# Optimization experiments

Hardware: AMD Instinct MI355X
Metric: run time of the kernel (lower is better)

## Reference

```python
import jax, jax.numpy as jnp
import numpy as np

N, D, K = 131072, 64, 1024


def setup_inputs() -> dict:
    key = jax.random.key(0)
    kx, kc = jax.random.split(key)
    x = jax.random.normal(kx, (N, D), dtype=jnp.float32)
    codebook = jax.random.normal(kc, (K, D), dtype=jnp.float32)
    return {"x": x, "codebook": codebook}


def reference(x, codebook):
    # Pairwise squared L2 distances, expanded form to avoid the [N, K, D]
    # intermediate the naive vmap would materialize:
    x_sq = jnp.sum(x * x, axis=-1, keepdims=True)            # [N, 1]
    c_sq = jnp.sum(codebook * codebook, axis=-1)             # [K]
    xc = jnp.einsum("nd,kd->nk", x, codebook)                # [N, K]
    l2_sum = x_sq - 2.0 * xc + c_sq[None, :]                 # [N, K]
    codes = jnp.argmin(l2_sum, axis=-1)                      # [N] int
    code_vec = jnp.take(codebook, codes, axis=0)             # [N, D]
    return (code_vec, codes, l2_sum)
```

## Files before the change

### kernel.cpp

```cpp
#include <hip/hip_runtime.h>
#include <stdint.h>

#define NROWS 131072
#define DDIM  64
#define KCB   1024
#define BM    128
#define NCHUNK 16
#define XPAD  68

typedef short bf16x8 __attribute__((ext_vector_type(8)));
typedef float f32x4  __attribute__((ext_vector_type(4)));

__device__ __forceinline__ unsigned short f2bf(float f) {
    unsigned int u = __float_as_uint(f);
    u += 0x7FFFu + ((u >> 16) & 1u);
    return (unsigned short)(u >> 16);
}
__device__ __forceinline__ float bf2f(unsigned short h) {
    return __uint_as_float(((unsigned int)h) << 16);
}

__global__ __launch_bounds__(256)
void convert_cb(const float* __restrict__ cb,
                unsigned short* __restrict__ mh,
                unsigned short* __restrict__ ml,
                float* __restrict__ csq) {
    const int t    = blockIdx.x * 256 + threadIdx.x;
    const int row  = t >> 2;
    const int part = t & 3;
    const float4* src = (const float4*)(cb + (size_t)row * DDIM + part * 16);

    unsigned short hb[16], lb[16];
    float s = 0.f;
#pragma unroll
    for (int q = 0; q < 4; ++q) {
        float4 v = src[q];
        float c, m; unsigned short h;
        c = v.x; s = fmaf(c, c, s); m = -2.f * c; h = f2bf(m);
        hb[q*4+0] = h; lb[q*4+0] = f2bf(m - bf2f(h));
        c = v.y; s = fmaf(c, c, s); m = -2.f * c; h = f2bf(m);
        hb[q*4+1] = h; lb[q*4+1] = f2bf(m - bf2f(h));
        c = v.z; s = fmaf(c, c, s); m = -2.f * c; h = f2bf(m);
        hb[q*4+2] = h; lb[q*4+2] = f2bf(m - bf2f(h));
        c = v.w; s = fmaf(c, c, s); m = -2.f * c; h = f2bf(m);
        hb[q*4+3] = h; lb[q*4+3] = f2bf(m - bf2f(h));
    }
    s += __shfl_xor(s, 1);
    s += __shfl_xor(s, 2);
    if (part == 0) csq[row] = s;

    const size_t off = (size_t)row * DDIM + part * 16;
    short4* dh = (short4*)(mh + off);
    short4* dl = (short4*)(ml + off);
#pragma unroll
    for (int q = 0; q < 4; ++q) {
        short4 hv, lv;
        hv.x = (short)hb[q*4+0]; hv.y = (short)hb[q*4+1];
        hv.z = (short)hb[q*4+2]; hv.w = (short)hb[q*4+3];
        lv.x = (short)lb[q*4+0]; lv.y = (short)lb[q*4+1];
        lv.z = (short)lb[q*4+2]; lv.w = (short)lb[q*4+3];
        dh[q] = hv; dl[q] = lv;
    }
}

__device__ __forceinline__ void cvt8(float4 f0, float4 f1, bf16x8* h, bf16x8* l) {
    bf16x8 hh, ll;
    float fv; unsigned short hb;
    fv = f0.x; hb = f2bf(fv); hh[0] = (short)hb; ll[0] = (short)f2bf(fv - bf2f(hb));
    fv = f0.y; hb = f2bf(fv); hh[1] = (short)hb; ll[1] = (short)f2bf(fv - bf2f(hb));
    fv = f0.z; hb = f2bf(fv); hh[2] = (short)hb; ll[2] = (short)f2bf(fv - bf2f(hb));
    fv = f0.w; hb = f2bf(fv); hh[3] = (short)hb; ll[3] = (short)f2bf(fv - bf2f(hb));
    fv = f1.x; hb = f2bf(fv); hh[4] = (short)hb; ll[4] = (short)f2bf(fv - bf2f(hb));
    fv = f1.y; hb = f2bf(fv); hh[5] = (short)hb; ll[5] = (short)f2bf(fv - bf2f(hb));
    fv = f1.z; hb = f2bf(fv); hh[6] = (short)hb; ll[6] = (short)f2bf(fv - bf2f(hb));
    fv = f1.w; hb = f2bf(fv); hh[7] = (short)hb; ll[7] = (short)f2bf(fv - bf2f(hb));
    *h = hh; *l = ll;
}

__global__ __launch_bounds__(256, 4)
void codebook_mfma(const float* __restrict__ x,
                   const float* __restrict__ cb,
                   const unsigned short* __restrict__ cbh,
                   const unsigned short* __restrict__ cbl,
                   const float* __restrict__ csq,
                   float* __restrict__ out_codevec,
                   float* __restrict__ out_codes,
                   float* __restrict__ out_l2) {
    __shared__ float xs[BM][XPAD];
    __shared__ float xsq_s[BM];
    __shared__ int   cand_s[BM][2];

    const int tid  = threadIdx.x;
    const int lane = tid & 63;
    const int wid  = tid >> 6;
    const int row0 = blockIdx.x * BM;

    {
        const int r = tid >> 1, h = tid & 1;
        const float4* src = (const float4*)(x + (size_t)(row0 + r) * DDIM + h * 32);
        float4* dst = (float4*)&xs[r][h * 32];
        float s0 = 0.f, s1 = 0.f;
#pragma unroll
        for (int q = 0; q < 8; ++q) {
            float4 v = src[q];
            dst[q] = v;
            s0 = fmaf(v.x, v.x, s0); s0 = fmaf(v.y, v.y, s0);
            s1 = fmaf(v.z, v.z, s1); s1 = fmaf(v.w, v.w, s1);
        }
        float s = s0 + s1;
        s += __shfl_xor(s, 1);
        if (h == 0) xsq_s[r] = s;
    }
    __syncthreads();

    const int mrow = wid * 32;
    const int cl   = lane & 15;
    const int ch   = lane >> 4;

    bf16x8 xh[2][2], xl[2][2];
#pragma unroll
    for (int mt = 0; mt < 2; ++mt)
#pragma unroll
    for (int ks = 0; ks < 2; ++ks) {
        const float* p = &xs[mrow + mt * 16 + cl][ks * 32 + ch * 8];
        cvt8(*(const float4*)p, *(const float4*)(p + 4), &xh[mt][ks], &xl[mt][ks]);
    }

    float xq[2];
    xq[0] = xsq_s[mrow + cl];
    xq[1] = xsq_s[mrow + 16 + cl];

    float m1[2], m2[2];
    int   i1[2], i2[2];
#pragma unroll
    for (int mt = 0; mt < 2; ++mt) {
        m1[mt] = 3.4e38f; m2[mt] = 3.4e38f; i1[mt] = 0; i2[mt] = 0;
    }

    for (int chunk = 0; chunk < NCHUNK; ++chunk) {
        const int k0 = chunk << 6;

#pragma unroll
        for (int nt = 0; nt < 4; ++nt) {
            const int ncol = k0 + nt * 16 + cl;
            const size_t bof = (size_t)ncol * DDIM + ch * 8;
            const bf16x8 bh0 = *(const bf16x8*)(cbh + bof);
            const bf16x8 bh1 = *(const bf16x8*)(cbh + bof + 32);
            const bf16x8 bl0 = *(const bf16x8*)(cbl + bof);
            const bf16x8 bl1 = *(const bf16x8*)(cbl + bof + 32);
            const f32x4  cqv = *(const f32x4*)(csq + k0 + nt * 16 + ch * 4);

#pragma unroll
            for (int mt = 0; mt < 2; ++mt) {
                f32x4 a;
                a[0] = xq[mt] + cqv[0]; a[1] = xq[mt] + cqv[1];
                a[2] = xq[mt] + cqv[2]; a[3] = xq[mt] + cqv[3];
                a = __builtin_amdgcn_mfma_f32_16x16x32_bf16(bh0, xh[mt][0], a, 0, 0, 0);
                a = __builtin_amdgcn_mfma_f32_16x16x32_bf16(bh1, xh[mt][1], a, 0, 0, 0);
                a = __builtin_amdgcn_mfma_f32_16x16x32_bf16(bh0, xl[mt][0], a, 0, 0, 0);
                a = __builtin_amdgcn_mfma_f32_16x16x32_bf16(bh1, xl[mt][1], a, 0, 0, 0);
                a = __builtin_amdgcn_mfma_f32_16x16x32_bf16(bl0, xh[mt][0], a, 0, 0, 0);
                a = __builtin_amdgcn_mfma_f32_16x16x32_bf16(bl1, xh[mt][1], a, 0, 0, 0);

                f32x4* dst = (f32x4*)(out_l2 +
                    (size_t)(row0 + mrow + mt * 16 + cl) * KCB + k0 + nt * 16 + ch * 4);
                *dst = a;

                const int idx0 = k0 + nt * 16 + ch * 4;
#pragma unroll
                for (int rg = 0; rg < 4; ++rg) {
                    const float v = a[rg];
                    const int idx = idx0 + rg;
                    const bool c1 = v < m1[mt];
                    const bool c2 = v < m2[mt];
                    const float nm2 = c1 ? m1[mt] : (c2 ? v : m2[mt]);
                    const int   ni2 = c1 ? i1[mt] : (c2 ? idx : i2[mt]);
                    m2[mt] = nm2; i2[mt] = ni2;
                    m1[mt] = c1 ? v : m1[mt];
                    i1[mt] = c1 ? idx : i1[mt];
                }
            }
        }
    }

#pragma unroll
    for (int mt = 0; mt < 2; ++mt) {
        float a1 = m1[mt], a2 = m2[mt];
        int   j1 = i1[mt], j2 = i2[mt];
#pragma unroll
        for (int mm = 16; mm <= 32; mm <<= 1) {
            float o1 = __shfl_xor(a1, mm), o2 = __shfl_xor(a2, mm);
            int   q1 = __shfl_xor(j1, mm), q2 = __shfl_xor(j2, mm);
            const bool fw = (o1 < a1) || (o1 == a1 && q1 < j1);
            const float w1 = fw ? o1 : a1; const int wj1 = fw ? q1 : j1;
            const float ca = fw ? a1 : o1; const int cja = fw ? j1 : q1;
            const float cbv = fw ? o2 : a2; const int cjb = fw ? q2 : j2;
            const bool sw = (cbv < ca) || (cbv == ca && cjb < cja);
            a1 = w1; j1 = wj1;
            a2 = sw ? cbv : ca; j2 = sw ? cjb : cja;
        }
        if (ch == 0) {
            const int r = mrow + mt * 16 + cl;
            cand_s[r][0] = j1; cand_s[r][1] = j2;
        }
    }
    __syncthreads();

    {
        const int r = tid >> 1, h = tid & 1;
        const int cand = cand_s[r][h];
        const float4* xr = (const float4*)&xs[r][0];
        const float4* cr = (const float4*)(cb + (size_t)cand * DDIM);
        float s0 = 0.f, s1 = 0.f, s2 = 0.f, s3 = 0.f;
#pragma unroll
        for (int q = 0; q < 4; ++q) {
            float4 xa, ca;
            xa = xr[q];      ca = cr[q];
            s0 = fmaf(xa.x, ca.x, s0); s0 = fmaf(xa.y, ca.y, s0);
            s0 = fmaf(xa.z, ca.z, s0); s0 = fmaf(xa.w, ca.w, s0);
            xa = xr[q + 4];  ca = cr[q + 4];
            s1 = fmaf(xa.x, ca.x, s1); s1 = fmaf(xa.y, ca.y, s1);
            s1 = fmaf(xa.z, ca.z, s1); s1 = fmaf(xa.w, ca.w, s1);
            xa = xr[q + 8];  ca = cr[q + 8];
            s2 = fmaf(xa.x, ca.x, s2); s2 = fmaf(xa.y, ca.y, s2);
            s2 = fmaf(xa.z, ca.z, s2); s2 = fmaf(xa.w, ca.w, s2);
            xa = xr[q + 12]; ca = cr[q + 12];
            s3 = fmaf(xa.x, ca.x, s3); s3 = fmaf(xa.y, ca.y, s3);
            s3 = fmaf(xa.z, ca.z, s3); s3 = fmaf(xa.w, ca.w, s3);
        }
        const float dot = (s0 + s1) + (s2 + s3);
        const float d = fmaf(-2.f, dot, xsq_s[r] + csq[cand]);
        const float od = __shfl_xor(d, 1);
        const int   oc = __shfl_xor(cand, 1);
        const bool win = (d < od) || (d == od && cand < oc);
        const int w = win ? cand : oc;
        if (h == 0) out_codes[row0 + r] = (float)w;
        const float4* wv = (const float4*)(cb + (size_t)w * DDIM + h * 32);
        float4* ov = (float4*)(out_codevec + (size_t)(row0 + r) * DDIM + h * 32);
#pragma unroll
        for (int q = 0; q < 8; ++q) ov[q] = wv[q];
    }
}

extern "C" void kernel_launch(void* const* d_in, const int* in_sizes, int n_in,
                              void* d_out, int out_size, void* d_ws, size_t ws_size,
                              hipStream_t stream) {
    (void)in_sizes; (void)n_in; (void)out_size; (void)ws_size;
    const float* x  = (const float*)d_in[0];
    const float* cb = (const float*)d_in[1];

    unsigned short* cbh = (unsigned short*)d_ws;
    unsigned short* cbl = cbh + (size_t)KCB * DDIM;
    float*          csq = (float*)(cbl + (size_t)KCB * DDIM);

    float* out_codevec = (float*)d_out;
    float* out_codes   = out_codevec + (size_t)NROWS * DDIM;
    float* out_l2      = out_codes + NROWS;

    convert_cb<<<16, 256, 0, stream>>>(cb, cbh, cbl, csq);
    codebook_mfma<<<NROWS / BM, 256, 0, stream>>>(x, cb, cbh, cbl, csq,
                                                  out_codevec, out_codes, out_l2);
}
```

Measured before the change: 256.8 us.

## Halve row tile per block and batch L2 stores per 256-column group

Shrinks the block tile from 128 to 64 rows so each wave handles a single 16-row MFMA tile, which doubles the number of blocks while each block still reads the full codebook. Accumulators for 256 codebook columns are held in registers and written to the L2 output in a burst after each group instead of right after each tile's MFMAs. The epilogue is respread over four threads per row. The aim is more parallelism and better-grouped output stores, at the cost of twice the codebook reads per row and higher register pressure, with occupancy lowered to 3 waves in launch bounds.

```diff
diff --git a/kernel.cpp b/kernel.cpp
--- a/kernel.cpp
+++ b/kernel.cpp
@@ -4,8 +4,7 @@
 #define NROWS 131072
 #define DDIM  64
 #define KCB   1024
-#define BM    128
-#define NCHUNK 16
+#define BM    64
 #define XPAD  68
 
 typedef short bf16x8 __attribute__((ext_vector_type(8)));
@@ -77,7 +76,7 @@
     *h = hh; *l = ll;
 }
 
-__global__ __launch_bounds__(256, 4)
+__global__ __launch_bounds__(256, 3)
 void codebook_mfma(const float* __restrict__ x,
                    const float* __restrict__ cb,
                    const unsigned short* __restrict__ cbh,
@@ -96,12 +95,12 @@
     const int row0 = blockIdx.x * BM;
 
     {
-        const int r = tid >> 1, h = tid & 1;
-        const float4* src = (const float4*)(x + (size_t)(row0 + r) * DDIM + h * 32);
-        float4* dst = (float4*)&xs[r][h * 32];
+        const int r = tid >> 2, p = tid & 3;
+        const float4* src = (const float4*)(x + (size_t)(row0 + r) * DDIM + p * 16);
+        float4* dst = (float4*)&xs[r][p * 16];
         float s0 = 0.f, s1 = 0.f;
 #pragma unroll
-        for (int q = 0; q < 8; ++q) {
+        for (int q = 0; q < 4; ++q) {
             float4 v = src[q];
             dst[q] = v;
             s0 = fmaf(v.x, v.x, s0); s0 = fmaf(v.y, v.y, s0);
@@ -109,84 +108,84 @@
         }
         float s = s0 + s1;
         s += __shfl_xor(s, 1);
-        if (h == 0) xsq_s[r] = s;
+        s += __shfl_xor(s, 2);
+        if (p == 0) xsq_s[r] = s;
     }
     __syncthreads();
 
-    const int mrow = wid * 32;
+    const int wrow = wid * 16;
     const int cl   = lane & 15;
     const int ch   = lane >> 4;
 
-    bf16x8 xh[2][2], xl[2][2];
-#pragma unroll
-    for (int mt = 0; mt < 2; ++mt)
+    bf16x8 xh[2], xl[2];
 #pragma unroll
     for (int ks = 0; ks < 2; ++ks) {
-        const float* p = &xs[mrow + mt * 16 + cl][ks * 32 + ch * 8];
-        cvt8(*(const float4*)p, *(const float4*)(p + 4), &xh[mt][ks], &xl[mt][ks]);
-    }
-
-    float xq[2];
-    xq[0] = xsq_s[mrow + cl];
-    xq[1] = xsq_s[mrow + 16 + cl];
-
-    float m1[2], m2[2];
-    int   i1[2], i2[2];
-#pragma unroll
-    for (int mt = 0; mt < 2; ++mt) {
-        m1[mt] = 3.4e38f; m2[mt] = 3.4e38f; i1[mt] = 0; i2[mt] = 0;
-    }
-
-    for (int chunk = 0; chunk < NCHUNK; ++chunk) {
-        const int k0 = chunk << 6;
-
-#pragma unroll
-        for (int nt = 0; nt < 4; ++nt) {
-            const int ncol = k0 + nt * 16 + cl;
-            const size_t bof = (size_t)ncol * DDIM + ch * 8;
-            const bf16x8 bh0 = *(const bf16x8*)(cbh + bof);
-            const bf16x8 bh1 = *(const bf16x8*)(cbh + bof + 32);
-            const bf16x8 bl0 = *(const bf16x8*)(cbl + bof);
-            const bf16x8 bl1 = *(const bf16x8*)(cbl + bof + 32);
-            const f32x4  cqv = *(const f32x4*)(csq + k0 + nt * 16 + ch * 4);
-
-#pragma unroll
-            for (int mt = 0; mt < 2; ++mt) {
+        const float* p = &xs[wrow + cl][ks * 32 + ch * 8];
+        cvt8(*(const float4*)p, *(const float4*)(p + 4), &xh[ks], &xl[ks]);
+    }
+    const float xq = xsq_s[wrow + cl];
+
+    float m1 = 3.4e38f, m2 = 3.4e38f;
+    int   i1 = 0, i2 = 0;
+
+    const size_t rowbase = (size_t)(row0 + wrow + cl) * KCB;
+
+#pragma unroll
+    for (int g = 0; g < 4; ++g) {
+        f32x4 acc[4][4];
+
+#pragma unroll
+        for (int c = 0; c < 4; ++c) {
+            const int k0 = (g * 4 + c) << 6;
+#pragma unroll
+            for (int nt = 0; nt < 4; ++nt) {
+                const int ncol = k0 + nt * 16 + cl;
+                const size_t bof = (size_t)ncol * DDIM + ch * 8;
+                const bf16x8 bh0 = *(const bf16x8*)(cbh + bof);
+                const bf16x8 bh1 = *(const bf16x8*)(cbh + bof + 32);
+                const bf16x8 bl0 = *(const bf16x8*)(cbl + bof);
+                const bf16x8 bl1 = *(const bf16x8*)(cbl + bof + 32);
+                const f32x4  cqv = *(const f32x4*)(csq + k0 + nt * 16 + ch * 4);
+
                 f32x4 a;
-                a[0] = xq[mt] + cqv[0]; a[1] = xq[mt] + cqv[1];
-                a[2] = xq[mt] + cqv[2]; a[3] = xq[mt] + cqv[3];
-                a = __builtin_amdgcn_mfma_f32_16x16x32_bf16(bh0, xh[mt][0], a, 0, 0, 0);
-                a = __builtin_amdgcn_mfma_f32_16x16x32_bf16(bh1, xh[mt][1], a, 0, 0, 0);
-                a = __builtin_amdgcn_mfma_f32_16x16x32_bf16(bh0, xl[mt][0], a, 0, 0, 0);
-                a = __builtin_amdgcn_mfma_f32_16x16x32_bf16(bh1, xl[mt][1], a, 0, 0, 0);
-                a = __builtin_amdgcn_mfma_f32_16x16x32_bf16(bl0, xh[mt][0], a, 0, 0, 0);
-                a = __builtin_amdgcn_mfma_f32_16x16x32_bf16(bl1, xh[mt][1], a, 0, 0, 0);
-
-                f32x4* dst = (f32x4*)(out_l2 +
-                    (size_t)(row0 + mrow + mt * 16 + cl) * KCB + k0 + nt * 16 + ch * 4);
-                *dst = a;
+                a[0] = xq + cqv[0]; a[1] = xq + cqv[1];
+                a[2] = xq + cqv[2]; a[3] = xq + cqv[3];
+                a = __builtin_amdgcn_mfma_f32_16x16x32_bf16(bh0, xh[0], a, 0, 0, 0);
+                a = __builtin_amdgcn_mfma_f32_16x16x32_bf16(bh1, xh[1], a, 0, 0, 0);
+                a = __builtin_amdgcn_mfma_f32_16x16x32_bf16(bh0, xl[0], a, 0, 0, 0);
+                a = __builtin_amdgcn_mfma_f32_16x16x32_bf16(bh1, xl[1], a, 0, 0, 0);
+                a = __builtin_amdgcn_mfma_f32_16x16x32_bf16(bl0, xh[0], a, 0, 0, 0);
+                a = __builtin_amdgcn_mfma_f32_16x16x32_bf16(bl1, xh[1], a, 0, 0, 0);
+                acc[c][nt] = a;
 
                 const int idx0 = k0 + nt * 16 + ch * 4;
 #pragma unroll
                 for (int rg = 0; rg < 4; ++rg) {
                     const float v = a[rg];
                     const int idx = idx0 + rg;
-                    const bool c1 = v < m1[mt];
-                    const bool c2 = v < m2[mt];
-                    const float nm2 = c1 ? m1[mt] : (c2 ? v : m2[mt]);
-                    const int   ni2 = c1 ? i1[mt] : (c2 ? idx : i2[mt]);
-                    m2[mt] = nm2; i2[mt] = ni2;
-                    m1[mt] = c1 ? v : m1[mt];
-                    i1[mt] = c1 ? idx : i1[mt];
+                    const bool c1 = v < m1;
+                    const bool c2 = v < m2;
+                    const float nm2 = c1 ? m1 : (c2 ? v : m2);
+                    const int   ni2 = c1 ? i1 : (c2 ? idx : i2);
+                    m2 = nm2; i2 = ni2;
+                    m1 = c1 ? v : m1;
+                    i1 = c1 ? idx : i1;
                 }
             }
         }
-    }
-
-#pragma unroll
-    for (int mt = 0; mt < 2; ++mt) {
-        float a1 = m1[mt], a2 = m2[mt];
-        int   j1 = i1[mt], j2 = i2[mt];
+
+#pragma unroll
+        for (int c = 0; c < 4; ++c)
+#pragma unroll
+        for (int nt = 0; nt < 4; ++nt) {
+            f32x4* dst = (f32x4*)(out_l2 + rowbase + g * 256 + c * 64 + nt * 16 + ch * 4);
+            *dst = acc[c][nt];
+        }
+    }
+
+    {
+        float a1 = m1, a2 = m2;
+        int   j1 = i1, j2 = i2;
 #pragma unroll
         for (int mm = 16; mm <= 32; mm <<= 1) {
             float o1 = __shfl_xor(a1, mm), o2 = __shfl_xor(a2, mm);
@@ -200,45 +199,41 @@
             a2 = sw ? cbv : ca; j2 = sw ? cjb : cja;
         }
         if (ch == 0) {
-            const int r = mrow + mt * 16 + cl;
-            cand_s[r][0] = j1; cand_s[r][1] = j2;
+            cand_s[wrow + cl][0] = j1; cand_s[wrow + cl][1] = j2;
         }
     }
     __syncthreads();
 
     {
-        const int r = tid >> 1, h = tid & 1;
-        const int cand = cand_s[r][h];
-        const float4* xr = (const float4*)&xs[r][0];
-        const float4* cr = (const float4*)(cb + (size_t)cand * DDIM);
-        float s0 = 0.f, s1 = 0.f, s2 = 0.f, s3 = 0.f;
+        const int r = tid >> 2, p = tid & 3;
+        const int half = p & 1;
+        const int cnd  = p >> 1;
+        const int cand = cand_s[r][cnd];
+        const float4* xr = (const float4*)&xs[r][half * 32];
+        const float4* cr = (const float4*)(cb + (size_t)cand * DDIM + half * 32);
+        float s0 = 0.f, s1 = 0.f;
 #pragma unroll
         for (int q = 0; q < 4; ++q) {
             float4 xa, ca;
-            xa = xr[q];      ca = cr[q];
+            xa = xr[q];     ca = cr[q];
             s0 = fmaf(xa.x, ca.x, s0); s0 = fmaf(xa.y, ca.y, s0);
             s0 = fmaf(xa.z, ca.z, s0); s0 = fmaf(xa.w, ca.w, s0);
-            xa = xr[q + 4];  ca = cr[q + 4];
+            xa = xr[q + 4]; ca = cr[q + 4];
             s1 = fmaf(xa.x, ca.x, s1); s1 = fmaf(xa.y, ca.y, s1);
             s1 = fmaf(xa.z, ca.z, s1); s1 = fmaf(xa.w, ca.w, s1);
-            xa = xr[q + 8];  ca = cr[q + 8];
-            s2 = fmaf(xa.x, ca.x, s2); s2 = fmaf(xa.y, ca.y, s2);
-            s2 = fmaf(xa.z, ca.z, s2); s2 = fmaf(xa.w, ca.w, s2);
-            xa = xr[q + 12]; ca = cr[q + 12];
-            s3 = fmaf(xa.x, ca.x, s3); s3 = fmaf(xa.y, ca.y, s3);
-            s3 = fmaf(xa.z, ca.z, s3); s3 = fmaf(xa.w, ca.w, s3);
-        }
-        const float dot = (s0 + s1) + (s2 + s3);
+        }
+        float dot = s0 + s1;
+        dot += __shfl_xor(dot, 1);
         const float d = fmaf(-2.f, dot, xsq_s[r] + csq[cand]);
-        const float od = __shfl_xor(d, 1);
-        const int   oc = __shfl_xor(cand, 1);
+        const float od = __shfl_xor(d, 2);
+        const int   oc = __shfl_xor(cand, 2);
         const bool win = (d < od) || (d == od && cand < oc);
         const int w = win ? cand : oc;
-        if (h == 0) out_codes[row0 + r] = (float)w;
-        const float4* wv = (const float4*)(cb + (size_t)w * DDIM + h * 32);
-        float4* ov = (float4*)(out_codevec + (size_t)(row0 + r) * DDIM + h * 32);
-#pragma unroll
-        for (int q = 0; q < 8; ++q) ov[q] = wv[q];
+        if (p == 0) out_codes[row0 + r] = (float)w;
+        const float4* wv = (const float4*)(cb + (size_t)w * DDIM + p * 16);
+        float4* ov = (float4*)(out_codevec + (size_t)(row0 + r) * DDIM + p * 16);
+#pragma unroll
+        for (int q = 0; q < 4; ++q) ov[q] = wv[q];
     }
 }
 
```

Result: slower. 308.9 us (+20.3%).

## Double-buffer codebook register loads with sched barriers to overlap MFMA compute

Applied to the files above, without the earlier changes.

Restructures the main loop into 32 steps of 32 codebook columns and uses two register buffers (A/B) so the codebook hi/lo and c_sq loads for the next step are issued before computing the current one. Scheduling barriers pin this order so the compiler cannot merge loads and compute. The aim is to hide global/L2 load latency behind MFMA and argmin work. Doubling the register buffers raises VGPR use, so launch bounds drop from 4 to 3 blocks per SM, which costs occupancy.

```diff
diff --git a/kernel.cpp b/kernel.cpp
--- a/kernel.cpp
+++ b/kernel.cpp
@@ -5,7 +5,7 @@
 #define DDIM  64
 #define KCB   1024
 #define BM    128
-#define NCHUNK 16
+#define NSTEP 32
 #define XPAD  68
 
 typedef short bf16x8 __attribute__((ext_vector_type(8)));
@@ -77,7 +77,67 @@
     *h = hh; *l = ll;
 }
 
-__global__ __launch_bounds__(256, 4)
+__device__ __forceinline__ void prefetch_step(
+        int hh, int cl, int ch,
+        const unsigned short* __restrict__ cbh,
+        const unsigned short* __restrict__ cbl,
+        const float* __restrict__ csq,
+        bf16x8 (&bh0)[2], bf16x8 (&bh1)[2],
+        bf16x8 (&bl0)[2], bf16x8 (&bl1)[2], f32x4 (&cq)[2]) {
+#pragma unroll
+    for (int nt2 = 0; nt2 < 2; ++nt2) {
+        const int ncol = hh * 32 + nt2 * 16 + cl;
+        const size_t bof = (size_t)ncol * DDIM + ch * 8;
+        bh0[nt2] = *(const bf16x8*)(cbh + bof);
+        bh1[nt2] = *(const bf16x8*)(cbh + bof + 32);
+        bl0[nt2] = *(const bf16x8*)(cbl + bof);
+        bl1[nt2] = *(const bf16x8*)(cbl + bof + 32);
+        cq[nt2]  = *(const f32x4*)(csq + hh * 32 + nt2 * 16 + ch * 4);
+    }
+}
+
+__device__ __forceinline__ void compute_step(
+        int hh, int cl, int ch, size_t outbase0, size_t outbase1,
+        const bf16x8 (&bh0)[2], const bf16x8 (&bh1)[2],
+        const bf16x8 (&bl0)[2], const bf16x8 (&bl1)[2], const f32x4 (&cq)[2],
+        const bf16x8 (&xh)[2][2], const bf16x8 (&xl)[2][2], const float (&xq)[2],
+        float (&m1)[2], float (&m2)[2], int (&i1)[2], int (&i2)[2],
+        float* __restrict__ out_l2) {
+#pragma unroll
+    for (int nt2 = 0; nt2 < 2; ++nt2) {
+#pragma unroll
+        for (int mt = 0; mt < 2; ++mt) {
+            f32x4 a;
+            a[0] = xq[mt] + cq[nt2][0]; a[1] = xq[mt] + cq[nt2][1];
+            a[2] = xq[mt] + cq[nt2][2]; a[3] = xq[mt] + cq[nt2][3];
+            a = __builtin_amdgcn_mfma_f32_16x16x32_bf16(bh0[nt2], xh[mt][0], a, 0, 0, 0);
+            a = __builtin_amdgcn_mfma_f32_16x16x32_bf16(bh1[nt2], xh[mt][1], a, 0, 0, 0);
+            a = __builtin_amdgcn_mfma_f32_16x16x32_bf16(bh0[nt2], xl[mt][0], a, 0, 0, 0);
+            a = __builtin_amdgcn_mfma_f32_16x16x32_bf16(bh1[nt2], xl[mt][1], a, 0, 0, 0);
+            a = __builtin_amdgcn_mfma_f32_16x16x32_bf16(bl0[nt2], xh[mt][0], a, 0, 0, 0);
+            a = __builtin_amdgcn_mfma_f32_16x16x32_bf16(bl1[nt2], xh[mt][1], a, 0, 0, 0);
+
+            const int coff = hh * 32 + nt2 * 16 + ch * 4;
+            f32x4* dst = (f32x4*)(out_l2 + (mt == 0 ? outbase0 : outbase1) + coff);
+            *dst = a;
+
+#pragma unroll
+            for (int rg = 0; rg < 4; ++rg) {
+                const float v = a[rg];
+                const int idx = coff + rg;
+                const bool c1 = v < m1[mt];
+                const bool c2 = v < m2[mt];
+                const float nm2 = c1 ? m1[mt] : (c2 ? v : m2[mt]);
+                const int   ni2 = c1 ? i1[mt] : (c2 ? idx : i2[mt]);
+                m2[mt] = nm2; i2[mt] = ni2;
+                m1[mt] = c1 ? v : m1[mt];
+                i1[mt] = c1 ? idx : i1[mt];
+            }
+        }
+    }
+}
+
+__global__ __launch_bounds__(256, 3)
 void codebook_mfma(const float* __restrict__ x,
                    const float* __restrict__ cb,
                    const unsigned short* __restrict__ cbh,
@@ -137,50 +197,28 @@
         m1[mt] = 3.4e38f; m2[mt] = 3.4e38f; i1[mt] = 0; i2[mt] = 0;
     }
 
-    for (int chunk = 0; chunk < NCHUNK; ++chunk) {
-        const int k0 = chunk << 6;
-
-#pragma unroll
-        for (int nt = 0; nt < 4; ++nt) {
-            const int ncol = k0 + nt * 16 + cl;
-            const size_t bof = (size_t)ncol * DDIM + ch * 8;
-            const bf16x8 bh0 = *(const bf16x8*)(cbh + bof);
-            const bf16x8 bh1 = *(const bf16x8*)(cbh + bof + 32);
-            const bf16x8 bl0 = *(const bf16x8*)(cbl + bof);
-            const bf16x8 bl1 = *(const bf16x8*)(cbl + bof + 32);
-            const f32x4  cqv = *(const f32x4*)(csq + k0 + nt * 16 + ch * 4);
-
-#pragma unroll
-            for (int mt = 0; mt < 2; ++mt) {
-                f32x4 a;
-                a[0] = xq[mt] + cqv[0]; a[1] = xq[mt] + cqv[1];
-                a[2] = xq[mt] + cqv[2]; a[3] = xq[mt] + cqv[3];
-                a = __builtin_amdgcn_mfma_f32_16x16x32_bf16(bh0, xh[mt][0], a, 0, 0, 0);
-                a = __builtin_amdgcn_mfma_f32_16x16x32_bf16(bh1, xh[mt][1], a, 0, 0, 0);
-                a = __builtin_amdgcn_mfma_f32_16x16x32_bf16(bh0, xl[mt][0], a, 0, 0, 0);
-                a = __builtin_amdgcn_mfma_f32_16x16x32_bf16(bh1, xl[mt][1], a, 0, 0, 0);
-                a = __builtin_amdgcn_mfma_f32_16x16x32_bf16(bl0, xh[mt][0], a, 0, 0, 0);
-                a = __builtin_amdgcn_mfma_f32_16x16x32_bf16(bl1, xh[mt][1], a, 0, 0, 0);
-
-                f32x4* dst = (f32x4*)(out_l2 +
-                    (size_t)(row0 + mrow + mt * 16 + cl) * KCB + k0 + nt * 16 + ch * 4);
-                *dst = a;
-
-                const int idx0 = k0 + nt * 16 + ch * 4;
-#pragma unroll
-                for (int rg = 0; rg < 4; ++rg) {
-                    const float v = a[rg];
-                    const int idx = idx0 + rg;
-                    const bool c1 = v < m1[mt];
-                    const bool c2 = v < m2[mt];
-                    const float nm2 = c1 ? m1[mt] : (c2 ? v : m2[mt]);
-                    const int   ni2 = c1 ? i1[mt] : (c2 ? idx : i2[mt]);
-                    m2[mt] = nm2; i2[mt] = ni2;
-                    m1[mt] = c1 ? v : m1[mt];
-                    i1[mt] = c1 ? idx : i1[mt];
-                }
-            }
-        }
+    const size_t outbase0 = (size_t)(row0 + mrow + cl) * KCB;
+    const size_t outbase1 = (size_t)(row0 + mrow + 16 + cl) * KCB;
+
+    bf16x8 Abh0[2], Abh1[2], Abl0[2], Abl1[2]; f32x4 Acq[2];
+    bf16x8 Bbh0[2], Bbh1[2], Bbl0[2], Bbl1[2]; f32x4 Bcq[2];
+
+    prefetch_step(0, cl, ch, cbh, cbl, csq, Abh0, Abh1, Abl0, Abl1, Acq);
+
+    for (int h = 0; h < NSTEP; h += 2) {
+        prefetch_step(h + 1, cl, ch, cbh, cbl, csq, Bbh0, Bbh1, Bbl0, Bbl1, Bcq);
+        __builtin_amdgcn_sched_barrier(0);
+        compute_step(h, cl, ch, outbase0, outbase1,
+                     Abh0, Abh1, Abl0, Abl1, Acq,
+                     xh, xl, xq, m1, m2, i1, i2, out_l2);
+        __builtin_amdgcn_sched_barrier(0);
+        if (h + 2 < NSTEP)
+            prefetch_step(h + 2, cl, ch, cbh, cbl, csq, Abh0, Abh1, Abl0, Abl1, Acq);
+        __builtin_amdgcn_sched_barrier(0);
+        compute_step(h + 1, cl, ch, outbase0, outbase1,
+                     Bbh0, Bbh1, Bbl0, Bbl1, Bcq,
+                     xh, xl, xq, m1, m2, i1, i2, out_l2);
+        __builtin_amdgcn_sched_barrier(0);
     }
 
 #pragma unroll
```

New measurement: 230.0 us. 10.4% less time.
